# Performance work log

Hardware: AMD Instinct MI355X
Metric: run time of the kernel (lower is better)

Reference implementation:

```python
import jax, jax.numpy as jnp
import numpy as np
from jax import lax

B, S, D, H = 64, 512, 768, 1024

def setup_inputs() -> dict:
    key = jax.random.key(0)
    ks = jax.random.split(key, 11)
    s = 0.02
    return {
        "x":  jax.random.normal(ks[0], (B, S, D), jnp.float32),
        "Wm": jax.random.normal(ks[1], (H, D), jnp.float32) * s,  # markov: 768->1024
        "bm": jnp.zeros((H,), jnp.float32),
        "Wh": jax.random.normal(ks[2], (H, D), jnp.float32) * s,  # hc1: 768->1024
        "bh": jnp.zeros((H,), jnp.float32),
        "Wz": jax.random.normal(ks[3], (H, 2 * H), jnp.float32) * s,  # update gate
        "bz": jnp.zeros((H,), jnp.float32),
        "Wr": jax.random.normal(ks[4], (H, 2 * H), jnp.float32) * s,  # reset gate
        "br": jnp.zeros((H,), jnp.float32),
        "Wi": jax.random.normal(ks[5], (H, 2 * H), jnp.float32) * s,  # candidate gate
        "bi": jnp.zeros((H,), jnp.float32),
    }


def reference(x, Wm, bm, Wh, bh, Wz, bz, Wr, br, Wi, bi):
    # initial hidden = hc1(first token), shape [B, H]
    h0 = x[:, 0, :] @ Wh.T + bh
    # markov projection batched over all timesteps: [B, S, H]
    u = jnp.einsum("bsd,hd->bsh", x, Wm) + bm

    def step(h, u_t):  # h: [B,H], u_t: [B,H]
        comb = jnp.concatenate([u_t, h], axis=-1)          # [B, 2H]
        z = jax.nn.sigmoid(comb @ Wz.T + bz)
        r = jax.nn.sigmoid(comb @ Wr.T + br)
        comb_r = jnp.concatenate([u_t, r * h], axis=-1)    # [B, 2H]
        h_prime = jnp.tanh(comb_r @ Wi.T + bi)
        h_new = (1.0 - z) * h + z * h_prime
        return h_new, None

    h_final, _ = lax.scan(step, h0, jnp.swapaxes(u, 0, 1))  # scan over S
    return h_final[:, None, :]  # [B, 1, H]
```

## Files before the change

### kernel.cpp

```cpp
#include <hip/hip_runtime.h>
#include <hip/hip_bf16.h>
#include <stdint.h>


#define B_  64
#define S_  512
#define D_  768
#define H_  1024

typedef __attribute__((ext_vector_type(8))) short short8;
typedef __attribute__((ext_vector_type(4))) float f32x4;
typedef __attribute__((ext_vector_type(4))) unsigned short u16x4;

static __device__ __forceinline__ short f2bf(float f) {
  union { float f; uint32_t u; } v; v.f = f;
  uint32_t u = v.u;
  u += 0x7FFFu + ((u >> 16) & 1u);
  return (short)(u >> 16);
}
static __device__ __forceinline__ float bf2f(short s) {
  union { uint32_t u; float f; } v; v.u = ((uint32_t)(uint16_t)s) << 16;
  return v.f;
}
static __device__ __forceinline__ void load_lds16(const void* g, void* l) {
  __builtin_amdgcn_global_load_lds((const __attribute__((address_space(1))) void*)g,
                                   (__attribute__((address_space(3))) void*)l, 16, 0, 0);
}

static __device__ __forceinline__ short8 load_frag_sys(const short* p) {
  short8 v;
  asm volatile("global_load_dwordx4 %0, %1, off sc0 sc1" : "=v"(v) : "v"(p));
  return v;
}
static __device__ __forceinline__ void atomic_store64(void* p, uint64_t v) {
  asm volatile("global_atomic_swap_x2 %0, %1, off" :: "v"(p), "v"(v) : "memory");
}
static __device__ __forceinline__ void atomic_store32(uint32_t* p, uint32_t v) {
  asm volatile("global_atomic_swap %0, %1, off" :: "v"(p), "v"(v) : "memory");
}
static __device__ __forceinline__ void wait_vm0() {
  asm volatile("s_waitcnt vmcnt(0)" ::: "memory");
  __builtin_amdgcn_sched_barrier(0);
}
static __device__ __forceinline__ void barrier_lds() {
  asm volatile("s_waitcnt lgkmcnt(0)" ::: "memory");
  __builtin_amdgcn_s_barrier();
  __builtin_amdgcn_sched_barrier(0);
}
static __device__ __forceinline__ void poll16(const uint32_t* base, uint32_t target) {
  const uint32_t* addr = base + ((threadIdx.x & 15) << 4);
  for (;;) {
    uint32_t v;
    asm volatile("global_load_dword %0, %1, off sc0 sc1\n\ts_waitcnt vmcnt(0)"
                 : "=v"(v) : "v"(addr) : "memory");
    if (__all((int)(v >= target))) break;
  }
  __builtin_amdgcn_sched_barrier(0);
}


__global__ void cast_f32_bf16_kernel(const float* __restrict__ in, short* __restrict__ out, int n8) {
  int i = blockIdx.x * blockDim.x + threadIdx.x;
  int stride = gridDim.x * blockDim.x;
  for (; i < n8; i += stride) {
    const f32x4* p = (const f32x4*)(in + (size_t)i * 8);
    f32x4 a = p[0], b = p[1];
    short8 o;
    o[0] = f2bf(a[0]); o[1] = f2bf(a[1]); o[2] = f2bf(a[2]); o[3] = f2bf(a[3]);
    o[4] = f2bf(b[0]); o[5] = f2bf(b[1]); o[6] = f2bf(b[2]); o[7] = f2bf(b[3]);
    *(short8*)(out + (size_t)i * 8) = o;
  }
}

__global__ void pack_h0_kernel(const float* __restrict__ hf, short* __restrict__ hp) {
  int i = blockIdx.x * blockDim.x + threadIdx.x;
  int col = i & 15, row = (i >> 4) & 15, j = (i >> 8) & 63, g = i >> 14;
  hp[i] = f2bf(hf[(size_t)(16 * g + row) * 1024 + j * 16 + col]);
}

__global__ void build_wcat_kernel(const float* __restrict__ Wz, const float* __restrict__ Wr,
                                  const float* __restrict__ Wi, short* __restrict__ out) {
  int idx = blockIdx.x * blockDim.x + threadIdx.x;
  int n = idx >> 7;
  int k8 = (idx & 127) << 3;
  const float* src;
  if (n < 1024)       src = Wz + ((size_t)n << 11);
  else if (n < 2048)  src = Wr + ((size_t)(n - 1024) << 11);
  else                src = Wi + ((size_t)(n - 2048) << 11);
  const f32x4* p = (const f32x4*)(src + k8);
  f32x4 a = p[0], b = p[1];
  short8 o;
  o[0] = f2bf(a[0]); o[1] = f2bf(a[1]); o[2] = f2bf(a[2]); o[3] = f2bf(a[3]);
  o[4] = f2bf(b[0]); o[5] = f2bf(b[1]); o[6] = f2bf(b[2]); o[7] = f2bf(b[3]);
  *(short8*)(out + ((size_t)n << 10) + k8) = o;
}

__global__ void transpose_cast_kernel(const float* __restrict__ in, short* __restrict__ out) {
  __shared__ float tile[32][33];
  int x = (blockIdx.x << 5) + threadIdx.x;
  int y0 = (blockIdx.y << 5);
#pragma unroll
  for (int i = threadIdx.y; i < 32; i += 8)
    tile[i][threadIdx.x] = in[(size_t)(y0 + i) * 768 + x];
  __syncthreads();
  int ox = (blockIdx.y << 5) + threadIdx.x;
  int oy0 = (blockIdx.x << 5);
#pragma unroll
  for (int i = threadIdx.y; i < 32; i += 8)
    out[(size_t)(oy0 + i) * 1024 + ox] = f2bf(tile[threadIdx.x][i]);
}

__global__ void ccat_kernel(const float* __restrict__ Wz, const float* __restrict__ Wr,
                            const float* __restrict__ Wi, const float* __restrict__ bm,
                            const float* __restrict__ bz, const float* __restrict__ br,
                            const float* __restrict__ bi, float* __restrict__ ccat) {
  int w = (blockIdx.x * blockDim.x + threadIdx.x) >> 6;
  int lane = threadIdx.x & 63;
  if (w >= 3072) return;
  const float* src; const float* bsrc; int ln;
  if (w < 1024)      { src = Wz + ((size_t)w << 11);          bsrc = bz; ln = w; }
  else if (w < 2048) { src = Wr + ((size_t)(w - 1024) << 11); bsrc = br; ln = w - 1024; }
  else               { src = Wi + ((size_t)(w - 2048) << 11); bsrc = bi; ln = w - 2048; }
  float acc = 0.f;
  for (int k = lane; k < 1024; k += 64) acc += src[k] * bm[k];
  for (int off = 32; off > 0; off >>= 1) acc += __shfl_down(acc, off, 64);
  if (lane == 0) ccat[w] = acc + bsrc[ln];
}

__global__ void pack_w_kernel(const float* __restrict__ Wz, const float* __restrict__ Wr,
                              const float* __restrict__ Wi, short* __restrict__ out) {
  int idx = blockIdx.x * blockDim.x + threadIdx.x;
  int lane = idx & 63;
  int t8 = (idx >> 6) & 7;
  int w = (idx >> 9) & 3;
  int j = (idx >> 11) & 63;
  int m = idx >> 17;
  int colv = (j << 4) + (lane & 15);
  int k = 1024 + (w << 8) + (t8 << 5) + ((lane >> 4) << 3);
  const float* W = (m == 0) ? Wr : (m == 1) ? Wz : Wi;
  const float* p = W + ((size_t)colv << 11) + k;
  short8 o;
#pragma unroll
  for (int e = 0; e < 8; ++e) o[e] = f2bf(p[e]);
  *(short8*)(out + ((size_t)idx << 3)) = o;
}


template<bool OUT_F32>
__launch_bounds__(256, 2)
__global__ void gemm_nt_kernel(const short* __restrict__ A, long lda,
                               const short* __restrict__ Bm,
                               void* __restrict__ Cv, int ldc,
                               const float* __restrict__ bias,
                               int M, int N, int K) {
  __shared__ short ldsA[128 * 64];
  __shared__ short ldsB[128 * 64];
  const int tile_m = blockIdx.x << 7;
  const int tile_n = blockIdx.y << 7;
  const int tid = threadIdx.x;
  const int wave = tid >> 6;
  const int lane = tid & 63;
  const int wm = wave & 1;
  const int wn = wave >> 1;
  const int lrow = lane & 15;
  const int lgrp = lane >> 4;

  f32x4 acc[4][4];
#pragma unroll
  for (int a = 0; a < 4; ++a)
#pragma unroll
    for (int b = 0; b < 4; ++b) acc[a][b] = (f32x4){0.f, 0.f, 0.f, 0.f};

  for (int kt = 0; kt < K; kt += 64) {
    __syncthreads();
#pragma unroll
    for (int c = 0; c < 4; ++c) {
      int o = ((wave * 4 + c) << 10) + (lane << 4);
      int row = o >> 7;
      int cb = (o & 127) ^ ((row & 7) << 4);
      int grow = tile_m + row; if (grow >= M) grow = M - 1;
      load_lds16(A + (size_t)grow * lda + kt + (cb >> 1),
                 (char*)ldsA + ((wave * 4 + c) << 10));
      int gcol = tile_n + row;
      load_lds16(Bm + (size_t)gcol * K + kt + (cb >> 1),
                 (char*)ldsB + ((wave * 4 + c) << 10));
    }
    __syncthreads();
#pragma unroll
    for (int kk = 0; kk < 2; ++kk) {
      short8 af[4], bfr[4];
      int kb = (kk << 6) + (lgrp << 4);
#pragma unroll
      for (int a = 0; a < 4; ++a) {
        int r = (wm << 6) + (a << 4) + lrow;
        af[a] = *(const short8*)((const char*)ldsA + (r << 7) + (kb ^ ((r & 7) << 4)));
        int rn = (wn << 6) + (a << 4) + lrow;
        bfr[a] = *(const short8*)((const char*)ldsB + (rn << 7) + (kb ^ ((rn & 7) << 4)));
      }
#pragma unroll
      for (int a = 0; a < 4; ++a)
#pragma unroll
        for (int b = 0; b < 4; ++b)
          acc[a][b] = __builtin_amdgcn_mfma_f32_16x16x32_bf16(af[a], bfr[b], acc[a][b], 0, 0, 0);
    }
  }
#pragma unroll
  for (int a = 0; a < 4; ++a)
#pragma unroll
    for (int b = 0; b < 4; ++b)
#pragma unroll
      for (int q = 0; q < 4; ++q) {
        int r = tile_m + (wm << 6) + (a << 4) + lgrp * 4 + q;
        int cc = tile_n + (wn << 6) + (b << 4) + lrow;
        if (r < M) {
          float v = acc[a][b][q];
          if (bias) v += bias[cc];
          if (OUT_F32) ((float*)Cv)[(size_t)r * ldc + cc] = v;
          else         ((short*)Cv)[(size_t)r * ldc + cc] = f2bf(v);
        }
      }
}


__launch_bounds__(256, 1)
__global__ void recurrence_kernel(const short* __restrict__ pk,
                                  const short* __restrict__ Gcat,
                                  const float* __restrict__ hf,
                                  short* __restrict__ hp,
                                  short* __restrict__ rhp,
                                  uint32_t* __restrict__ flags,
                                  float* __restrict__ out) {
  __shared__ float red[3][4][320];
  const int blk = blockIdx.x;
  const int g = blk >> 6;
  const int j = blk & 63;
  const int tid = threadIdx.x;
  const int wave = tid >> 6;
  const int lane = tid & 63;
  const int lrow = lane & 15;
  const int lgrp = lane >> 4;
  const int m0 = g << 4;

  short8 wr[8], wz[8], wi[8];
  {
    const short8* p8 = (const short8*)pk;
    size_t base = ((size_t)j * 4 + wave) * 8;
#pragma unroll
    for (int t8 = 0; t8 < 8; ++t8) wr[t8] = p8[(base + t8) * 64 + lane];
#pragma unroll
    for (int t8 = 0; t8 < 8; ++t8) wz[t8] = p8[((size_t)2048 + base + t8) * 64 + lane];
#pragma unroll
    for (int t8 = 0; t8 < 8; ++t8) wi[t8] = p8[((size_t)4096 + base + t8) * 64 + lane];
  }

  uint32_t* fgrp = flags + (g << 11);

  const int row16 = lane >> 2;
  const int c4 = (lane & 3) << 2;
  float hold[4];
  float zv[4];
  if (wave == 0) {
#pragma unroll
    for (int c = 0; c < 4; ++c)
      hold[c] = hf[((size_t)(m0 + row16) << 10) + (j << 4) + c4 + c];
  }

  const size_t cbase = ((size_t)(g * 64) << 8);
  const int coff = ((16 * wave + (lgrp >> 1)) << 8) + (lrow << 4) + ((lgrp & 1) << 3);

  short* const prodRh = rhp + ((size_t)(g * 64 + j) << 8) + (row16 << 4) + c4;
  short* const prodH  = hp  + ((size_t)(g * 64 + j) << 8) + (row16 << 4) + c4;

  float gz[4], gr[4], gi[4], gzn[4], grn[4], gin[4];
  const unsigned short* GcatU = (const unsigned short*)Gcat;
  if (wave == 0) {
    size_t rbase = ((size_t)(m0 + row16) * S_) * 3072 + (j << 4) + c4;
    u16x4 vz = *(const u16x4*)(GcatU + rbase);
    u16x4 vr = *(const u16x4*)(GcatU + rbase + 1024);
    u16x4 vi = *(const u16x4*)(GcatU + rbase + 2048);
#pragma unroll
    for (int c = 0; c < 4; ++c) {
      gz[c] = bf2f((short)vz[c]); gr[c] = bf2f((short)vr[c]); gi[c] = bf2f((short)vi[c]);
    }
  }

  for (int t = 0; t < S_; ++t) {
    if (t > 0) poll16(fgrp + 1024 + (wave << 8), (uint32_t)t);
    short8 hfrag[8];
#pragma unroll
    for (int t8 = 0; t8 < 8; ++t8)
      hfrag[t8] = load_frag_sys(hp + cbase + coff + (t8 << 9));
    wait_vm0();
    f32x4 accr = (f32x4){0.f,0.f,0.f,0.f}, accz = (f32x4){0.f,0.f,0.f,0.f};
#pragma unroll
    for (int t8 = 0; t8 < 8; ++t8) {
      accr = __builtin_amdgcn_mfma_f32_16x16x32_bf16(hfrag[t8], wr[t8], accr, 0, 0, 0);
      accz = __builtin_amdgcn_mfma_f32_16x16x32_bf16(hfrag[t8], wz[t8], accz, 0, 0, 0);
    }
#pragma unroll
    for (int q = 0; q < 4; ++q) {
      red[0][wave][lane * 5 + q] = accr[q];
      red[1][wave][lane * 5 + q] = accz[q];
    }
    barrier_lds();
    if (wave == 0) {
      uint32_t packed[2] = {0u, 0u};
#pragma unroll
      for (int c = 0; c < 4; ++c) {
        int li = (((row16 >> 2) << 4) + c4 + c) * 5 + (row16 & 3);
        float sr = red[0][0][li] + red[0][1][li] + red[0][2][li] + red[0][3][li] + gr[c];
        float sz = red[1][0][li] + red[1][1][li] + red[1][2][li] + red[1][3][li] + gz[c];
        sr = fminf(fmaxf(sr, -30.f), 30.f);
        sz = fminf(fmaxf(sz, -30.f), 30.f);
        float rv = 1.f / (1.f + __expf(-sr));
        zv[c] = 1.f / (1.f + __expf(-sz));
        packed[c >> 1] |= ((uint32_t)(uint16_t)f2bf(rv * hold[c])) << ((c & 1) * 16);
      }
      atomic_store64(prodRh, ((uint64_t)packed[1] << 32) | packed[0]);
      wait_vm0();
      if (lane == 0) atomic_store32(fgrp + (j << 4), (uint32_t)(t + 1));
    }
    poll16(fgrp + (wave << 8), (uint32_t)(t + 1));
    u16x4 vz, vr, vi;
    if (wave == 0) {
      int tn = (t < S_ - 1) ? t + 1 : t;
      size_t rbase = ((size_t)(m0 + row16) * S_ + tn) * 3072 + (j << 4) + c4;
      vz = *(const u16x4*)(GcatU + rbase);
      vr = *(const u16x4*)(GcatU + rbase + 1024);
      vi = *(const u16x4*)(GcatU + rbase + 2048);
    }
    short8 rhfrag[8];
#pragma unroll
    for (int t8 = 0; t8 < 8; ++t8)
      rhfrag[t8] = load_frag_sys(rhp + cbase + coff + (t8 << 9));
    wait_vm0();
    f32x4 acci = (f32x4){0.f,0.f,0.f,0.f};
#pragma unroll
    for (int t8 = 0; t8 < 8; ++t8)
      acci = __builtin_amdgcn_mfma_f32_16x16x32_bf16(rhfrag[t8], wi[t8], acci, 0, 0, 0);
#pragma unroll
    for (int q = 0; q < 4; ++q) red[2][wave][lane * 5 + q] = acci[q];
    barrier_lds();
    if (wave == 0) {
      uint32_t packed[2] = {0u, 0u};
      float hn4[4];
#pragma unroll
      for (int c = 0; c < 4; ++c) {
        gzn[c] = bf2f((short)vz[c]); grn[c] = bf2f((short)vr[c]); gin[c] = bf2f((short)vi[c]);
      }
#pragma unroll
      for (int c = 0; c < 4; ++c) {
        int li = (((row16 >> 2) << 4) + c4 + c) * 5 + (row16 & 3);
        float si = red[2][0][li] + red[2][1][li] + red[2][2][li] + red[2][3][li] + gi[c];
        si = fminf(fmaxf(si, -30.f), 30.f);
        float e2 = __expf(2.f * si);
        float hp_ = (e2 - 1.f) / (e2 + 1.f);
        float hn = (1.f - zv[c]) * hold[c] + zv[c] * hp_;
        hold[c] = hn; hn4[c] = hn;
        packed[c >> 1] |= ((uint32_t)(uint16_t)f2bf(hn)) << ((c & 1) * 16);
      }
      atomic_store64(prodH, ((uint64_t)packed[1] << 32) | packed[0]);
      if (t == S_ - 1) {
#pragma unroll
        for (int c = 0; c < 4; ++c)
          out[((size_t)(m0 + row16) << 10) + (j << 4) + c4 + c] = hn4[c];
      }
      wait_vm0();
      if (lane == 0) atomic_store32(fgrp + 1024 + (j << 4), (uint32_t)(t + 1));
#pragma unroll
      for (int c = 0; c < 4; ++c) { gz[c] = gzn[c]; gr[c] = grn[c]; gi[c] = gin[c]; }
    }
  }
}


extern "C" void kernel_launch(void* const* d_in, const int* in_sizes, int n_in,
                              void* d_out, int out_size, void* d_ws, size_t ws_size,
                              hipStream_t stream) {
  const float* x  = (const float*)d_in[0];
  const float* Wm = (const float*)d_in[1];
  const float* bm = (const float*)d_in[2];
  const float* Wh = (const float*)d_in[3];
  const float* bh = (const float*)d_in[4];
  const float* Wz = (const float*)d_in[5];
  const float* bz = (const float*)d_in[6];
  const float* Wr = (const float*)d_in[7];
  const float* br = (const float*)d_in[8];
  const float* Wi = (const float*)d_in[9];
  const float* bi = (const float*)d_in[10];

  char* ws = (char*)d_ws;
  size_t off = 0;
  auto alloc = [&](size_t bytes) -> void* {
    void* p = ws + off; off += (bytes + 255) & ~(size_t)255; return p;
  };
  short* xbf   = (short*)alloc((size_t)B_ * S_ * D_ * 2);
  short* Gcat  = (short*)alloc((size_t)B_ * S_ * 3072 * 2);
  short* Mcat  = (short*)alloc((size_t)3072 * 768 * 2);
  short* Wcat  = (short*)alloc((size_t)3072 * 1024 * 2);
  short* WmT   = (short*)alloc((size_t)768 * 1024 * 2);
  short* Whbf  = (short*)alloc((size_t)1024 * 768 * 2);
  short* pk    = (short*)alloc((size_t)3 * 1024 * 1024 * 2);
  float* ccat  = (float*)alloc(3072 * 4);
  float* hf    = (float*)alloc(65536 * 4);
  short* hp    = (short*)alloc(65536 * 2);
  short* rhp   = (short*)alloc(65536 * 2);
  uint32_t* flags = (uint32_t*)alloc((size_t)4 * 2048 * 4);
  if (off > ws_size) return;

  hipMemsetAsync(flags, 0, (size_t)4 * 2048 * 4, stream);
  cast_f32_bf16_kernel<<<2048, 256, 0, stream>>>(x, xbf, (B_ * S_ * D_) / 8);
  cast_f32_bf16_kernel<<<384, 256, 0, stream>>>(Wh, Whbf, (1024 * 768) / 8);
  build_wcat_kernel<<<1536, 256, 0, stream>>>(Wz, Wr, Wi, Wcat);
  transpose_cast_kernel<<<dim3(24, 32), dim3(32, 8), 0, stream>>>(Wm, WmT);
  ccat_kernel<<<768, 256, 0, stream>>>(Wz, Wr, Wi, bm, bz, br, bi, ccat);
  pack_w_kernel<<<1536, 256, 0, stream>>>(Wz, Wr, Wi, pk);

  gemm_nt_kernel<false><<<dim3(24, 6), 256, 0, stream>>>(Wcat, 1024, WmT, Mcat, 768,
                                                         nullptr, 3072, 768, 1024);
  gemm_nt_kernel<false><<<dim3(256, 24), 256, 0, stream>>>(xbf, 768, Mcat, Gcat, 3072,
                                                           ccat, 32768, 3072, 768);
  gemm_nt_kernel<true><<<dim3(1, 8), 256, 0, stream>>>(xbf, (long)S_ * D_, Whbf, hf, 1024,
                                                       bh, 64, 1024, 768);
  pack_h0_kernel<<<256, 256, 0, stream>>>(hf, hp);

  recurrence_kernel<<<256, 256, 0, stream>>>(pk, Gcat, hf, hp, rhp, flags,
                                             (float*)d_out);
}
```

Before: 3.002 ms.

## Collapse batch groups into one 64-block recurrence with pipelined fragment loads

The persistent recurrence kernel drops from 256 blocks (4 batch groups × 64 column slices) to 64 blocks. Each block now handles all 64 batch rows, and every wave finalizes its own 16 rows instead of wave 0 doing all the gate math. The hidden-state fragment loads are split into four double-buffered chunks that overlap with the MFMAs, and the flag set shrinks to one group. The aim is to cut the number of blocks polling flags and to spread the elementwise work across all waves. In exchange each block performs four times as many MFMAs and loads per step, and fewer CUs take part.

Measured after the change: 3.934 ms. 1.31x slower.

```diff
diff --git a/kernel.cpp b/kernel.cpp
--- a/kernel.cpp
+++ b/kernel.cpp
@@ -27,16 +27,16 @@
                                    (__attribute__((address_space(3))) void*)l, 16, 0, 0);
 }
 
-static __device__ __forceinline__ short8 load_frag_sys(const short* p) {
-  short8 v;
-  asm volatile("global_load_dwordx4 %0, %1, off sc0 sc1" : "=v"(v) : "v"(p));
-  return v;
-}
 static __device__ __forceinline__ void atomic_store64(void* p, uint64_t v) {
   asm volatile("global_atomic_swap_x2 %0, %1, off" :: "v"(p), "v"(v) : "memory");
 }
 static __device__ __forceinline__ void atomic_store32(uint32_t* p, uint32_t v) {
   asm volatile("global_atomic_swap %0, %1, off" :: "v"(p), "v"(v) : "memory");
+}
+static __device__ __forceinline__ u16x4 load_g8(const unsigned short* p) {
+  u16x4 v;
+  asm volatile("global_load_dwordx2 %0, %1, off" : "=v"(v) : "v"(p));
+  return v;
 }
 static __device__ __forceinline__ void wait_vm0() {
   asm volatile("s_waitcnt vmcnt(0)" ::: "memory");
@@ -57,6 +57,28 @@
   }
   __builtin_amdgcn_sched_barrier(0);
 }
+
+#define ISSUE8(buf, src, eoff)                                                    \
+  _Pragma("unroll")                                                               \
+  for (int t8_ = 0; t8_ < 8; ++t8_)                                               \
+    asm volatile("global_load_dwordx4 %0, %1, off sc0 sc1"                        \
+                 : "=v"(buf[t8_]) : "v"((src) + (eoff) + t8_ * 2048));
+
+#define WAITV(n)                                                                  \
+  asm volatile("s_waitcnt vmcnt(" #n ")" ::: "memory");                           \
+  __builtin_amdgcn_sched_barrier(0);
+
+#define MFMA_RZ(buf, ar, az)                                                      \
+  _Pragma("unroll")                                                               \
+  for (int t8_ = 0; t8_ < 8; ++t8_) {                                             \
+    ar = __builtin_amdgcn_mfma_f32_16x16x32_bf16(buf[t8_], wr[t8_], ar, 0, 0, 0); \
+    az = __builtin_amdgcn_mfma_f32_16x16x32_bf16(buf[t8_], wz[t8_], az, 0, 0, 0); \
+  }
+
+#define MFMA_I(buf, ai)                                                           \
+  _Pragma("unroll")                                                               \
+  for (int t8_ = 0; t8_ < 8; ++t8_)                                               \
+    ai = __builtin_amdgcn_mfma_f32_16x16x32_bf16(buf[t8_], wi[t8_], ai, 0, 0, 0);
 
 
 __global__ void cast_f32_bf16_kernel(const float* __restrict__ in, short* __restrict__ out, int n8) {
@@ -74,8 +96,8 @@
 
 __global__ void pack_h0_kernel(const float* __restrict__ hf, short* __restrict__ hp) {
   int i = blockIdx.x * blockDim.x + threadIdx.x;
-  int col = i & 15, row = (i >> 4) & 15, j = (i >> 8) & 63, g = i >> 14;
-  hp[i] = f2bf(hf[(size_t)(16 * g + row) * 1024 + j * 16 + col]);
+  int col = i & 15, row = (i >> 4) & 63, j = i >> 10;
+  hp[i] = f2bf(hf[(size_t)row * 1024 + j * 16 + col]);
 }
 
 __global__ void build_wcat_kernel(const float* __restrict__ Wz, const float* __restrict__ Wr,
@@ -230,16 +252,13 @@
                                   short* __restrict__ rhp,
                                   uint32_t* __restrict__ flags,
                                   float* __restrict__ out) {
-  __shared__ float red[3][4][320];
-  const int blk = blockIdx.x;
-  const int g = blk >> 6;
-  const int j = blk & 63;
+  __shared__ float red[3][4][4][320];
+  const int j = blockIdx.x;
   const int tid = threadIdx.x;
   const int wave = tid >> 6;
   const int lane = tid & 63;
   const int lrow = lane & 15;
   const int lgrp = lane >> 4;
-  const int m0 = g << 4;
 
   short8 wr[8], wz[8], wi[8];
   {
@@ -253,28 +272,26 @@
     for (int t8 = 0; t8 < 8; ++t8) wi[t8] = p8[((size_t)4096 + base + t8) * 64 + lane];
   }
 
-  uint32_t* fgrp = flags + (g << 11);
-
   const int row16 = lane >> 2;
   const int c4 = (lane & 3) << 2;
-  float hold[4];
-  float zv[4];
-  if (wave == 0) {
-#pragma unroll
-    for (int c = 0; c < 4; ++c)
-      hold[c] = hf[((size_t)(m0 + row16) << 10) + (j << 4) + c4 + c];
-  }
-
-  const size_t cbase = ((size_t)(g * 64) << 8);
-  const int coff = ((16 * wave + (lgrp >> 1)) << 8) + (lrow << 4) + ((lgrp & 1) << 3);
-
-  short* const prodRh = rhp + ((size_t)(g * 64 + j) << 8) + (row16 << 4) + c4;
-  short* const prodH  = hp  + ((size_t)(g * 64 + j) << 8) + (row16 << 4) + c4;
-
-  float gz[4], gr[4], gi[4], gzn[4], grn[4], gin[4];
+  const int erow = wave * 16 + row16;
+  float hold[4], zv[4];
+#pragma unroll
+  for (int c = 0; c < 4; ++c)
+    hold[c] = hf[(size_t)erow * 1024 + (j << 4) + c4 + c];
+
+  const int jbase = 16 * wave + (lgrp >> 1);
+  const int cbase0 = jbase * 1024 + lrow * 16 + ((lgrp & 1) << 3);
+  const short* hpc  = hp  + cbase0;
+  const short* rhpc = rhp + cbase0;
+
+  short* const prodRh = rhp + j * 1024 + erow * 16 + c4;
+  short* const prodH  = hp  + j * 1024 + erow * 16 + c4;
+
+  float gz[4], gr[4], gi[4];
   const unsigned short* GcatU = (const unsigned short*)Gcat;
-  if (wave == 0) {
-    size_t rbase = ((size_t)(m0 + row16) * S_) * 3072 + (j << 4) + c4;
+  {
+    size_t rbase = ((size_t)erow * S_) * 3072 + (j << 4) + c4;
     u16x4 vz = *(const u16x4*)(GcatU + rbase);
     u16x4 vr = *(const u16x4*)(GcatU + rbase + 1024);
     u16x4 vi = *(const u16x4*)(GcatU + rbase + 2048);
@@ -285,31 +302,39 @@
   }
 
   for (int t = 0; t < S_; ++t) {
-    if (t > 0) poll16(fgrp + 1024 + (wave << 8), (uint32_t)t);
-    short8 hfrag[8];
-#pragma unroll
-    for (int t8 = 0; t8 < 8; ++t8)
-      hfrag[t8] = load_frag_sys(hp + cbase + coff + (t8 << 9));
-    wait_vm0();
-    f32x4 accr = (f32x4){0.f,0.f,0.f,0.f}, accz = (f32x4){0.f,0.f,0.f,0.f};
-#pragma unroll
-    for (int t8 = 0; t8 < 8; ++t8) {
-      accr = __builtin_amdgcn_mfma_f32_16x16x32_bf16(hfrag[t8], wr[t8], accr, 0, 0, 0);
-      accz = __builtin_amdgcn_mfma_f32_16x16x32_bf16(hfrag[t8], wz[t8], accz, 0, 0, 0);
-    }
+    if (t > 0) poll16(flags + 1024 + (wave << 8), (uint32_t)t);
+    short8 fa[8], fb[8];
+    f32x4 accr0 = (f32x4){0,0,0,0}, accr1 = accr0, accr2 = accr0, accr3 = accr0;
+    f32x4 accz0 = accr0, accz1 = accr0, accz2 = accr0, accz3 = accr0;
+    ISSUE8(fa, hpc, 0);
+    ISSUE8(fb, hpc, 256);
+    WAITV(8);
+    MFMA_RZ(fa, accr0, accz0);
+    ISSUE8(fa, hpc, 512);
+    WAITV(8);
+    MFMA_RZ(fb, accr1, accz1);
+    ISSUE8(fb, hpc, 768);
+    WAITV(8);
+    MFMA_RZ(fa, accr2, accz2);
+    WAITV(0);
+    MFMA_RZ(fb, accr3, accz3);
 #pragma unroll
     for (int q = 0; q < 4; ++q) {
-      red[0][wave][lane * 5 + q] = accr[q];
-      red[1][wave][lane * 5 + q] = accz[q];
+      red[0][wave][0][lane * 5 + q] = accr0[q]; red[1][wave][0][lane * 5 + q] = accz0[q];
+      red[0][wave][1][lane * 5 + q] = accr1[q]; red[1][wave][1][lane * 5 + q] = accz1[q];
+      red[0][wave][2][lane * 5 + q] = accr2[q]; red[1][wave][2][lane * 5 + q] = accz2[q];
+      red[0][wave][3][lane * 5 + q] = accr3[q]; red[1][wave][3][lane * 5 + q] = accz3[q];
     }
     barrier_lds();
-    if (wave == 0) {
+    {
       uint32_t packed[2] = {0u, 0u};
 #pragma unroll
       for (int c = 0; c < 4; ++c) {
         int li = (((row16 >> 2) << 4) + c4 + c) * 5 + (row16 & 3);
-        float sr = red[0][0][li] + red[0][1][li] + red[0][2][li] + red[0][3][li] + gr[c];
-        float sz = red[1][0][li] + red[1][1][li] + red[1][2][li] + red[1][3][li] + gz[c];
+        float sr = red[0][0][wave][li] + red[0][1][wave][li] +
+                   red[0][2][wave][li] + red[0][3][wave][li] + gr[c];
+        float sz = red[1][0][wave][li] + red[1][1][wave][li] +
+                   red[1][2][wave][li] + red[1][3][wave][li] + gz[c];
         sr = fminf(fmaxf(sr, -30.f), 30.f);
         sz = fminf(fmaxf(sz, -30.f), 30.f);
         float rv = 1.f / (1.f + __expf(-sr));
@@ -317,41 +342,48 @@
         packed[c >> 1] |= ((uint32_t)(uint16_t)f2bf(rv * hold[c])) << ((c & 1) * 16);
       }
       atomic_store64(prodRh, ((uint64_t)packed[1] << 32) | packed[0]);
-      wait_vm0();
-      if (lane == 0) atomic_store32(fgrp + (j << 4), (uint32_t)(t + 1));
-    }
-    poll16(fgrp + (wave << 8), (uint32_t)(t + 1));
-    u16x4 vz, vr, vi;
-    if (wave == 0) {
+    }
+    wait_vm0();
+    barrier_lds();
+    if (tid == 0) atomic_store32(flags + (j << 4), (uint32_t)(t + 1));
+    u16x4 vzn, vrn, vin;
+    {
       int tn = (t < S_ - 1) ? t + 1 : t;
-      size_t rbase = ((size_t)(m0 + row16) * S_ + tn) * 3072 + (j << 4) + c4;
-      vz = *(const u16x4*)(GcatU + rbase);
-      vr = *(const u16x4*)(GcatU + rbase + 1024);
-      vi = *(const u16x4*)(GcatU + rbase + 2048);
-    }
-    short8 rhfrag[8];
-#pragma unroll
-    for (int t8 = 0; t8 < 8; ++t8)
-      rhfrag[t8] = load_frag_sys(rhp + cbase + coff + (t8 << 9));
-    wait_vm0();
-    f32x4 acci = (f32x4){0.f,0.f,0.f,0.f};
-#pragma unroll
-    for (int t8 = 0; t8 < 8; ++t8)
-      acci = __builtin_amdgcn_mfma_f32_16x16x32_bf16(rhfrag[t8], wi[t8], acci, 0, 0, 0);
-#pragma unroll
-    for (int q = 0; q < 4; ++q) red[2][wave][lane * 5 + q] = acci[q];
+      size_t rbase = ((size_t)erow * S_ + tn) * 3072 + (j << 4) + c4;
+      vzn = load_g8(GcatU + rbase);
+      vrn = load_g8(GcatU + rbase + 1024);
+      vin = load_g8(GcatU + rbase + 2048);
+    }
+    poll16(flags + (wave << 8), (uint32_t)(t + 1));
+    f32x4 acci0 = (f32x4){0,0,0,0}, acci1 = acci0, acci2 = acci0, acci3 = acci0;
+    ISSUE8(fa, rhpc, 0);
+    ISSUE8(fb, rhpc, 256);
+    WAITV(8);
+    MFMA_I(fa, acci0);
+    ISSUE8(fa, rhpc, 512);
+    WAITV(8);
+    MFMA_I(fb, acci1);
+    ISSUE8(fb, rhpc, 768);
+    WAITV(8);
+    MFMA_I(fa, acci2);
+    WAITV(0);
+    MFMA_I(fb, acci3);
+#pragma unroll
+    for (int q = 0; q < 4; ++q) {
+      red[2][wave][0][lane * 5 + q] = acci0[q];
+      red[2][wave][1][lane * 5 + q] = acci1[q];
+      red[2][wave][2][lane * 5 + q] = acci2[q];
+      red[2][wave][3][lane * 5 + q] = acci3[q];
+    }
     barrier_lds();
-    if (wave == 0) {
+    {
       uint32_t packed[2] = {0u, 0u};
       float hn4[4];
 #pragma unroll
       for (int c = 0; c < 4; ++c) {
-        gzn[c] = bf2f((short)vz[c]); grn[c] = bf2f((short)vr[c]); gin[c] = bf2f((short)vi[c]);
-      }
-#pragma unroll
-      for (int c = 0; c < 4; ++c) {
         int li = (((row16 >> 2) << 4) + c4 + c) * 5 + (row16 & 3);
-        float si = red[2][0][li] + red[2][1][li] + red[2][2][li] + red[2][3][li] + gi[c];
+        float si = red[2][0][wave][li] + red[2][1][wave][li] +
+                   red[2][2][wave][li] + red[2][3][wave][li] + gi[c];
         si = fminf(fmaxf(si, -30.f), 30.f);
         float e2 = __expf(2.f * si);
         float hp_ = (e2 - 1.f) / (e2 + 1.f);
@@ -363,12 +395,15 @@
       if (t == S_ - 1) {
 #pragma unroll
         for (int c = 0; c < 4; ++c)
-          out[((size_t)(m0 + row16) << 10) + (j << 4) + c4 + c] = hn4[c];
+          out[(size_t)erow * 1024 + (j << 4) + c4 + c] = hn4[c];
       }
-      wait_vm0();
-      if (lane == 0) atomic_store32(fgrp + 1024 + (j << 4), (uint32_t)(t + 1));
-#pragma unroll
-      for (int c = 0; c < 4; ++c) { gz[c] = gzn[c]; gr[c] = grn[c]; gi[c] = gin[c]; }
+    }
+    wait_vm0();
+    barrier_lds();
+    if (tid == 0) atomic_store32(flags + 1024 + (j << 4), (uint32_t)(t + 1));
+#pragma unroll
+    for (int c = 0; c < 4; ++c) {
+      gz[c] = bf2f((short)vzn[c]); gr[c] = bf2f((short)vrn[c]); gi[c] = bf2f((short)vin[c]);
     }
   }
 }
@@ -405,10 +440,10 @@
   float* hf    = (float*)alloc(65536 * 4);
   short* hp    = (short*)alloc(65536 * 2);
   short* rhp   = (short*)alloc(65536 * 2);
-  uint32_t* flags = (uint32_t*)alloc((size_t)4 * 2048 * 4);
+  uint32_t* flags = (uint32_t*)alloc((size_t)2048 * 4);
   if (off > ws_size) return;
 
-  hipMemsetAsync(flags, 0, (size_t)4 * 2048 * 4, stream);
+  hipMemsetAsync(flags, 0, (size_t)2048 * 4, stream);
   cast_f32_bf16_kernel<<<2048, 256, 0, stream>>>(x, xbf, (B_ * S_ * D_) / 8);
   cast_f32_bf16_kernel<<<384, 256, 0, stream>>>(Wh, Whbf, (1024 * 768) / 8);
   build_wcat_kernel<<<1536, 256, 0, stream>>>(Wz, Wr, Wi, Wcat);
@@ -424,6 +459,6 @@
                                                        bh, 64, 1024, 768);
   pack_h0_kernel<<<256, 256, 0, stream>>>(hf, hp);
 
-  recurrence_kernel<<<256, 256, 0, stream>>>(pk, Gcat, hf, hp, rhp, flags,
-                                             (float*)d_out);
-}
+  recurrence_kernel<<<64, 256, 0, stream>>>(pk, Gcat, hf, hp, rhp, flags,
+                                            (float*)d_out);
+}
```
